# Performance work log

Hardware: AMD Instinct MI355X
Metric: run time of the kernel (lower is better)

The kernel has to match this reference:

```python
import jax, jax.numpy as jnp
import numpy as np

UFEAT_DIM = 512
EFEAT_DIM = 256
BATCH = 64
PNUM_UNIT = 1024
PNUM_ENEMY = 1024


def setup_inputs() -> dict:
    key = jax.random.key(0)
    k1, k2, k3, k4, k5 = jax.random.split(key, 5)
    ufeat = jax.random.normal(k1, (BATCH, PNUM_UNIT, UFEAT_DIM), dtype=jnp.float32)
    efeat = jax.random.normal(k2, (BATCH, PNUM_ENEMY, EFEAT_DIM), dtype=jnp.float32)
    num_enemy = jax.random.randint(k3, (BATCH,), 0, PNUM_ENEMY, dtype=jnp.int64)
    # weight_norm(Linear, dim=None): W = g * v / ||v||_F, g scalar
    v = jax.random.normal(k4, (EFEAT_DIM, UFEAT_DIM), dtype=jnp.float32) * (1.0 / np.sqrt(UFEAT_DIM))
    g = jnp.asarray(jnp.linalg.norm(v), dtype=jnp.float32)  # init g = ||v||
    b = jax.random.normal(k5, (EFEAT_DIM,), dtype=jnp.float32) * 0.01
    return {"ufeat": ufeat, "efeat": efeat, "num_enemy": num_enemy, "v": v, "g": g, "b": b}


def reference(ufeat, efeat, num_enemy, v, g, b):
    # weight-normed linear (dim=None -> Frobenius norm) + ReLU projection
    W = g * v / jnp.linalg.norm(v)                       # [efeat_dim, ufeat_dim]
    proj = jax.nn.relu(ufeat @ W.T + b)                  # [B, U, efeat_dim]
    # batched dot-product scores (fused matmul instead of repeat+mul+sum)
    norm = jnp.float32(np.sqrt(EFEAT_DIM))
    logit = jnp.einsum('bue,bne->bun', proj, efeat) / norm  # [B, U, N]
    # real-enemy mask: mask[b, n] = 1 iff n < num_enemy[b]
    mask = (jnp.arange(PNUM_ENEMY)[None, :] < num_enemy[:, None]).astype(logit.dtype)
    logit = logit - (1.0 - mask)[:, None, :] * 1e9       # masking bias (uniform if all masked)
    prob = jax.nn.softmax(logit, axis=2)
    return prob
```

## Files before the change

### kernel.cpp

```cpp
#include <hip/hip_runtime.h>
#include <hip/hip_bf16.h>

#define UF 512
#define EF 256
#define NB 64
#define NU 1024
#define NEN 1024

typedef __attribute__((ext_vector_type(8))) short short8;
typedef __attribute__((ext_vector_type(4))) float floatx4;

typedef unsigned short ushort_t;

__device__ inline short2 cvt2(float a, float b) {
    __hip_bfloat162 h = __float22bfloat162_rn(make_float2(a, b));
    union { __hip_bfloat162 h; short2 s; } u;
    u.h = h;
    return u.s;
}

__device__ inline short8 cvt8v(floatx4 x, floatx4 y) {
    union { short8 v; short2 s[4]; } u;
    u.s[0] = cvt2(x[0], x[1]);
    u.s[1] = cvt2(x[2], x[3]);
    u.s[2] = cvt2(y[0], y[1]);
    u.s[3] = cvt2(y[2], y[3]);
    return u.v;
}

__device__ inline ushort_t f2bfbits(float f) {
    unsigned u = __float_as_uint(f);
    u += 0x7FFFu + ((u >> 16) & 1u);
    return (ushort_t)(u >> 16);
}

__global__ void knorm(const float* __restrict__ v, float* __restrict__ ws0) {
    int t = blockIdx.x * 256 + threadIdx.x;
    float2 x = ((const float2*)v)[t];
    float s = x.x * x.x + x.y * x.y;
    #pragma unroll
    for (int m = 1; m < 64; m <<= 1) s += __shfl_xor(s, m);
    __shared__ float ls[4];
    int w = threadIdx.x >> 6;
    if ((threadIdx.x & 63) == 0) ls[w] = s;
    __syncthreads();
    if (threadIdx.x == 0) atomicAdd(ws0, ls[0] + ls[1] + ls[2] + ls[3]);
}

__global__ void kconv(const float* __restrict__ v, const float* __restrict__ g,
                      const float* __restrict__ ef, const float* __restrict__ ws0,
                      const int* __restrict__ nen,
                      ushort_t* __restrict__ wsW, ushort_t* __restrict__ wsE) {
    int bid = blockIdx.x;
    if (bid < 128) {
        int t = bid * 256 + threadIdx.x;
        float s = g[0] * rsqrtf(ws0[0]);
        float4 x = ((const float4*)v)[t];
        short2 a = cvt2(x.x * s, x.y * s);
        short2 b = cvt2(x.z * s, x.w * s);
        ushort4 o;
        o.x = (ushort_t)a.x; o.y = (ushort_t)a.y; o.z = (ushort_t)b.x; o.w = (ushort_t)b.y;
        ((ushort4*)wsW)[t] = o;
    } else {
        long t = (long)(bid - 128) * 256 + threadIdx.x;
        int row = (int)(t >> 6);
        int n = row & (NEN - 1);
        int b = row >> 10;
        if (n < nen[b]) {
            floatx4 x = __builtin_nontemporal_load((const floatx4*)ef + t);
            short2 a = cvt2(x[0], x[1]);
            short2 c = cvt2(x[2], x[3]);
            ushort4 o;
            o.x = (ushort_t)a.x; o.y = (ushort_t)a.y; o.z = (ushort_t)c.x; o.w = (ushort_t)c.y;
            ((ushort4*)wsE)[t] = o;
        }
    }
}

__launch_bounds__(256, 2)
__global__ void kfused(const float* __restrict__ A, const ushort_t* __restrict__ W,
                       const float* __restrict__ bias, const ushort_t* __restrict__ E,
                       const int* __restrict__ nen, float* __restrict__ out) {
    const int tid = threadIdx.x;
    const int w = tid >> 6, L = tid & 63;
    const int rA = L & 15, q = L >> 4;
    const int bid = blockIdx.x;
    const int b = bid >> 5;
    const int ut = bid & 31;
    const int ne = nen[b];

    __shared__ ushort_t Pl[32][256];
    __shared__ float lsum[4][32];

    {
        const long m0 = (long)b * NU + (long)ut * 32;
        floatx4 acc[2][4];
        #pragma unroll
        for (int m = 0; m < 2; m++)
            #pragma unroll
            for (int n = 0; n < 4; n++) acc[m][n] = (floatx4){0.f, 0.f, 0.f, 0.f};

        const float* a0 = A + (m0 + rA) * UF + q * 8;
        const float* a1 = A + (m0 + 16 + rA) * UF + q * 8;
        const ushort_t* wp[4];
        #pragma unroll
        for (int n = 0; n < 4; n++) wp[n] = W + (long)(w * 64 + n * 16 + rA) * UF + q * 8;

        floatx4 x0 = *(const floatx4*)(a0);
        floatx4 y0 = *(const floatx4*)(a0 + 4);
        floatx4 x1 = *(const floatx4*)(a1);
        floatx4 y1 = *(const floatx4*)(a1 + 4);

        #pragma unroll 2
        for (int s = 0; s < 16; s++) {
            const int ko = s * 32;
            short8 wf[4];
            #pragma unroll
            for (int n = 0; n < 4; n++) wf[n] = *(const short8*)(wp[n] + ko);
            short8 af0 = cvt8v(x0, y0);
            short8 af1 = cvt8v(x1, y1);
            if (s < 15) {
                x0 = *(const floatx4*)(a0 + ko + 32);
                y0 = *(const floatx4*)(a0 + ko + 36);
                x1 = *(const floatx4*)(a1 + ko + 32);
                y1 = *(const floatx4*)(a1 + ko + 36);
            }
            #pragma unroll
            for (int n = 0; n < 4; n++) {
                acc[0][n] = __builtin_amdgcn_mfma_f32_16x16x32_bf16(af0, wf[n], acc[0][n], 0, 0, 0);
                acc[1][n] = __builtin_amdgcn_mfma_f32_16x16x32_bf16(af1, wf[n], acc[1][n], 0, 0, 0);
            }
        }

        #pragma unroll
        for (int n = 0; n < 4; n++) {
            const int col = w * 64 + n * 16 + rA;
            const float bv = bias[col];
            #pragma unroll
            for (int m = 0; m < 2; m++) {
                #pragma unroll
                for (int i = 0; i < 4; i++) {
                    float val = acc[m][n][i] + bv;
                    val = fmaxf(val, 0.f);
                    Pl[m * 16 + q * 4 + i][col] = f2bfbits(val);
                }
            }
        }
    }
    __syncthreads();

    short8 af[2][8];
    #pragma unroll
    for (int t = 0; t < 2; t++)
        #pragma unroll
        for (int s = 0; s < 8; s++)
            af[t][s] = *(const short8*)&Pl[t * 16 + rA][s * 32 + q * 8];

    floatx4 acc[2][16];
    #pragma unroll
    for (int t = 0; t < 2; t++)
        #pragma unroll
        for (int ns = 0; ns < 16; ns++) acc[t][ns] = (floatx4){0.f, 0.f, 0.f, 0.f};
    float psum[2][4];
    #pragma unroll
    for (int t = 0; t < 2; t++)
        #pragma unroll
        for (int i = 0; i < 4; i++) psum[t][i] = 0.f;

    const ushort_t* erow = E + (long)(b * NEN + w * 16 + rA) * EF + q * 8;

    #pragma unroll
    for (int ns = 0; ns < 16; ns++) {
        const int col0 = ns * 64 + w * 16;
        if (col0 < ne) {
            const ushort_t* ep = erow + (long)ns * 64 * EF;
            floatx4 c0 = (floatx4){0.f, 0.f, 0.f, 0.f};
            floatx4 c1 = (floatx4){0.f, 0.f, 0.f, 0.f};
            #pragma unroll
            for (int h = 0; h < 2; h++) {
                short8 bf[4];
                #pragma unroll
                for (int s = 0; s < 4; s++) bf[s] = *(const short8*)(ep + (h * 4 + s) * 32);
                #pragma unroll
                for (int s = 0; s < 4; s++) {
                    c0 = __builtin_amdgcn_mfma_f32_16x16x32_bf16(af[0][h * 4 + s], bf[s], c0, 0, 0, 0);
                    c1 = __builtin_amdgcn_mfma_f32_16x16x32_bf16(af[1][h * 4 + s], bf[s], c1, 0, 0, 0);
                }
            }
            const int col = col0 + rA;
            const bool on = col < ne;
            #pragma unroll
            for (int i = 0; i < 4; i++) {
                float e0 = on ? __expf(c0[i] * 0.0625f) : 0.f;
                float e1 = on ? __expf(c1[i] * 0.0625f) : 0.f;
                c0[i] = e0; c1[i] = e1;
                psum[0][i] += e0; psum[1][i] += e1;
            }
            acc[0][ns] = c0;
            acc[1][ns] = c1;
        }
    }

    #pragma unroll
    for (int t = 0; t < 2; t++)
        #pragma unroll
        for (int i = 0; i < 4; i++) {
            float s = psum[t][i];
            s += __shfl_xor(s, 1);
            s += __shfl_xor(s, 2);
            s += __shfl_xor(s, 4);
            s += __shfl_xor(s, 8);
            psum[t][i] = s;
        }
    if (rA == 0) {
        #pragma unroll
        for (int t = 0; t < 2; t++)
            #pragma unroll
            for (int i = 0; i < 4; i++)
                lsum[w][t * 16 + q * 4 + i] = psum[t][i];
    }
    __syncthreads();

    float inv[2][4];
    #pragma unroll
    for (int t = 0; t < 2; t++)
        #pragma unroll
        for (int i = 0; i < 4; i++) {
            const int r = t * 16 + q * 4 + i;
            const float tot = lsum[0][r] + lsum[1][r] + lsum[2][r] + lsum[3][r];
            inv[t][i] = (ne > 0) ? (1.f / tot) : 0.f;
        }

    const float uni = 1.f / 1024.f;
    float* orow = out + ((long)(b * NU + ut * 32)) * (long)NEN + w * 16;
    #pragma unroll
    for (int ns = 0; ns < 16; ns++) {
        #pragma unroll
        for (int t = 0; t < 2; t++) {
            #pragma unroll
            for (int i = 0; i < 4; i++) {
                const int u = t * 16 + q * 4 + i;
                const float val = (ne == 0) ? uni : acc[t][ns][i] * inv[t][i];
                __builtin_nontemporal_store(val, &orow[(long)u * NEN + ns * 64 + rA]);
            }
        }
    }
}

extern "C" void kernel_launch(void* const* d_in, const int* in_sizes, int n_in,
                              void* d_out, int out_size, void* d_ws, size_t ws_size,
                              hipStream_t stream) {
    (void)in_sizes; (void)n_in; (void)out_size; (void)ws_size;
    const float* ufeat = (const float*)d_in[0];
    const float* efeat = (const float*)d_in[1];
    const int*   nen   = (const int*)d_in[2];
    const float* v     = (const float*)d_in[3];
    const float* g     = (const float*)d_in[4];
    const float* bias  = (const float*)d_in[5];
    float* out = (float*)d_out;

    float*    ws0 = (float*)d_ws;
    ushort_t* wsW = (ushort_t*)((char*)d_ws + 1024);
    ushort_t* wsE = (ushort_t*)((char*)d_ws + (1u << 20));

    hipMemsetAsync(d_ws, 0, 256, stream);
    knorm<<<256, 256, 0, stream>>>(v, ws0);
    kconv<<<16512, 256, 0, stream>>>(v, g, efeat, ws0, nen, wsW, wsE);
    kfused<<<2048, 256, 0, stream>>>(ufeat, wsW, bias, wsE, nen, out);
}
```

Measured before the change: 569.2 us.

## Store exp accumulators as fp16, double-buffer E loads, pad LDS rows

The kernel now keeps the per-tile exponentiated scores in packed fp16 pairs instead of fp32, halving that register array so the E-operand loads can be double-buffered: the next tile's B fragments are prefetched while the current tile's MFMAs run. The LDS projection buffer is padded from 256 to 264 columns to cut bank conflicts on the fragment reads. The fp16 numerators lose precision, and because the max is never subtracted, unmasked exp values can overflow the fp16 range.

```diff
diff --git a/kernel.cpp b/kernel.cpp
--- a/kernel.cpp
+++ b/kernel.cpp
@@ -9,6 +9,7 @@
 
 typedef __attribute__((ext_vector_type(8))) short short8;
 typedef __attribute__((ext_vector_type(4))) float floatx4;
+typedef __attribute__((ext_vector_type(2))) _Float16 half2v;
 
 typedef unsigned short ushort_t;
 
@@ -89,7 +90,7 @@
     const int ut = bid & 31;
     const int ne = nen[b];
 
-    __shared__ ushort_t Pl[32][256];
+    __shared__ ushort_t Pl[32][264];
     __shared__ float lsum[4][32];
 
     {
@@ -156,11 +157,14 @@
         for (int s = 0; s < 8; s++)
             af[t][s] = *(const short8*)&Pl[t * 16 + rA][s * 32 + q * 8];
 
-    floatx4 acc[2][16];
-    #pragma unroll
-    for (int t = 0; t < 2; t++)
-        #pragma unroll
-        for (int ns = 0; ns < 16; ns++) acc[t][ns] = (floatx4){0.f, 0.f, 0.f, 0.f};
+    half2v acc[2][16][2];
+    #pragma unroll
+    for (int t = 0; t < 2; t++)
+        #pragma unroll
+        for (int ns = 0; ns < 16; ns++) {
+            acc[t][ns][0] = (half2v){(_Float16)0.f, (_Float16)0.f};
+            acc[t][ns][1] = (half2v){(_Float16)0.f, (_Float16)0.f};
+        }
     float psum[2][4];
     #pragma unroll
     for (int t = 0; t < 2; t++)
@@ -168,24 +172,29 @@
         for (int i = 0; i < 4; i++) psum[t][i] = 0.f;
 
     const ushort_t* erow = E + (long)(b * NEN + w * 16 + rA) * EF + q * 8;
+
+    short8 bf[2][8];
+    if (w * 16 < ne) {
+        #pragma unroll
+        for (int s = 0; s < 8; s++) bf[0][s] = *(const short8*)(erow + s * 32);
+    }
 
     #pragma unroll
     for (int ns = 0; ns < 16; ns++) {
         const int col0 = ns * 64 + w * 16;
         if (col0 < ne) {
-            const ushort_t* ep = erow + (long)ns * 64 * EF;
+            const int cur = ns & 1;
+            if (ns < 15) {
+                const ushort_t* epn = erow + (long)(ns + 1) * 64 * EF;
+                #pragma unroll
+                for (int s = 0; s < 8; s++) bf[cur ^ 1][s] = *(const short8*)(epn + s * 32);
+            }
             floatx4 c0 = (floatx4){0.f, 0.f, 0.f, 0.f};
             floatx4 c1 = (floatx4){0.f, 0.f, 0.f, 0.f};
             #pragma unroll
-            for (int h = 0; h < 2; h++) {
-                short8 bf[4];
-                #pragma unroll
-                for (int s = 0; s < 4; s++) bf[s] = *(const short8*)(ep + (h * 4 + s) * 32);
-                #pragma unroll
-                for (int s = 0; s < 4; s++) {
-                    c0 = __builtin_amdgcn_mfma_f32_16x16x32_bf16(af[0][h * 4 + s], bf[s], c0, 0, 0, 0);
-                    c1 = __builtin_amdgcn_mfma_f32_16x16x32_bf16(af[1][h * 4 + s], bf[s], c1, 0, 0, 0);
-                }
+            for (int s = 0; s < 8; s++) {
+                c0 = __builtin_amdgcn_mfma_f32_16x16x32_bf16(af[0][s], bf[cur][s], c0, 0, 0, 0);
+                c1 = __builtin_amdgcn_mfma_f32_16x16x32_bf16(af[1][s], bf[cur][s], c1, 0, 0, 0);
             }
             const int col = col0 + rA;
             const bool on = col < ne;
@@ -193,11 +202,13 @@
             for (int i = 0; i < 4; i++) {
                 float e0 = on ? __expf(c0[i] * 0.0625f) : 0.f;
                 float e1 = on ? __expf(c1[i] * 0.0625f) : 0.f;
+                psum[0][i] += e0; psum[1][i] += e1;
                 c0[i] = e0; c1[i] = e1;
-                psum[0][i] += e0; psum[1][i] += e1;
-            }
-            acc[0][ns] = c0;
-            acc[1][ns] = c1;
+            }
+            acc[0][ns][0] = (half2v){(_Float16)c0[0], (_Float16)c0[1]};
+            acc[0][ns][1] = (half2v){(_Float16)c0[2], (_Float16)c0[3]};
+            acc[1][ns][0] = (half2v){(_Float16)c1[0], (_Float16)c1[1]};
+            acc[1][ns][1] = (half2v){(_Float16)c1[2], (_Float16)c1[3]};
         }
     }
 
@@ -240,7 +251,8 @@
             #pragma unroll
             for (int i = 0; i < 4; i++) {
                 const int u = t * 16 + q * 4 + i;
-                const float val = (ne == 0) ? uni : acc[t][ns][i] * inv[t][i];
+                const float num = (float)acc[t][ns][i >> 1][i & 1];
+                const float val = (ne == 0) ? uni : num * inv[t][i];
                 __builtin_nontemporal_store(val, &orow[(long)u * NEN + ns * 64 + rA]);
             }
         }
```

Measured after the change: 563.7 us. About the same (-1.0%).

## Halve row tile, store exp values as fp16, and stage output through LDS

Applied to the files above, without the earlier changes.

The fused kernel now processes 16 user rows per block instead of 32, doubling the grid and raising the launch-bounds occupancy target to 4 blocks per CU. Exponentiated scores are held as fp16 pairs to cut register pressure. Output is written through a shared-memory staging buffer, so each wave issues coalesced 16-byte nontemporal stores instead of scattered scalar ones. The trade-offs are that each E tile is now reloaded by twice as many blocks, fp16 storage loses precision on the unnormalized exp values, and the staging adds barriers.

```diff
diff --git a/kernel.cpp b/kernel.cpp
--- a/kernel.cpp
+++ b/kernel.cpp
@@ -9,6 +9,7 @@
 
 typedef __attribute__((ext_vector_type(8))) short short8;
 typedef __attribute__((ext_vector_type(4))) float floatx4;
+typedef __attribute__((ext_vector_type(2))) _Float16 half2v;
 
 typedef unsigned short ushort_t;
 
@@ -77,7 +78,7 @@
     }
 }
 
-__launch_bounds__(256, 2)
+__launch_bounds__(256, 4)
 __global__ void kfused(const float* __restrict__ A, const ushort_t* __restrict__ W,
                        const float* __restrict__ bias, const ushort_t* __restrict__ E,
                        const int* __restrict__ nen, float* __restrict__ out) {
@@ -85,31 +86,29 @@
     const int w = tid >> 6, L = tid & 63;
     const int rA = L & 15, q = L >> 4;
     const int bid = blockIdx.x;
-    const int b = bid >> 5;
-    const int ut = bid & 31;
+    const int b = bid >> 6;
+    const int ut = bid & 63;
     const int ne = nen[b];
 
-    __shared__ ushort_t Pl[32][256];
-    __shared__ float lsum[4][32];
+    __shared__ union ShMem {
+        ushort_t Pl[16][264];
+        float    Cl[16][260];
+    } sh;
+    __shared__ float lsum[4][16];
 
     {
-        const long m0 = (long)b * NU + (long)ut * 32;
-        floatx4 acc[2][4];
-        #pragma unroll
-        for (int m = 0; m < 2; m++)
-            #pragma unroll
-            for (int n = 0; n < 4; n++) acc[m][n] = (floatx4){0.f, 0.f, 0.f, 0.f};
+        const long m0 = (long)b * NU + (long)ut * 16;
+        floatx4 acc[4];
+        #pragma unroll
+        for (int n = 0; n < 4; n++) acc[n] = (floatx4){0.f, 0.f, 0.f, 0.f};
 
         const float* a0 = A + (m0 + rA) * UF + q * 8;
-        const float* a1 = A + (m0 + 16 + rA) * UF + q * 8;
         const ushort_t* wp[4];
         #pragma unroll
         for (int n = 0; n < 4; n++) wp[n] = W + (long)(w * 64 + n * 16 + rA) * UF + q * 8;
 
         floatx4 x0 = *(const floatx4*)(a0);
         floatx4 y0 = *(const floatx4*)(a0 + 4);
-        floatx4 x1 = *(const floatx4*)(a1);
-        floatx4 y1 = *(const floatx4*)(a1 + 4);
 
         #pragma unroll 2
         for (int s = 0; s < 16; s++) {
@@ -118,18 +117,13 @@
             #pragma unroll
             for (int n = 0; n < 4; n++) wf[n] = *(const short8*)(wp[n] + ko);
             short8 af0 = cvt8v(x0, y0);
-            short8 af1 = cvt8v(x1, y1);
             if (s < 15) {
                 x0 = *(const floatx4*)(a0 + ko + 32);
                 y0 = *(const floatx4*)(a0 + ko + 36);
-                x1 = *(const floatx4*)(a1 + ko + 32);
-                y1 = *(const floatx4*)(a1 + ko + 36);
-            }
-            #pragma unroll
-            for (int n = 0; n < 4; n++) {
-                acc[0][n] = __builtin_amdgcn_mfma_f32_16x16x32_bf16(af0, wf[n], acc[0][n], 0, 0, 0);
-                acc[1][n] = __builtin_amdgcn_mfma_f32_16x16x32_bf16(af1, wf[n], acc[1][n], 0, 0, 0);
-            }
+            }
+            #pragma unroll
+            for (int n = 0; n < 4; n++)
+                acc[n] = __builtin_amdgcn_mfma_f32_16x16x32_bf16(af0, wf[n], acc[n], 0, 0, 0);
         }
 
         #pragma unroll
@@ -137,35 +131,27 @@
             const int col = w * 64 + n * 16 + rA;
             const float bv = bias[col];
             #pragma unroll
-            for (int m = 0; m < 2; m++) {
-                #pragma unroll
-                for (int i = 0; i < 4; i++) {
-                    float val = acc[m][n][i] + bv;
-                    val = fmaxf(val, 0.f);
-                    Pl[m * 16 + q * 4 + i][col] = f2bfbits(val);
-                }
+            for (int i = 0; i < 4; i++) {
+                float val = acc[n][i] + bv;
+                val = fmaxf(val, 0.f);
+                sh.Pl[q * 4 + i][col] = f2bfbits(val);
             }
         }
     }
     __syncthreads();
 
-    short8 af[2][8];
-    #pragma unroll
-    for (int t = 0; t < 2; t++)
-        #pragma unroll
-        for (int s = 0; s < 8; s++)
-            af[t][s] = *(const short8*)&Pl[t * 16 + rA][s * 32 + q * 8];
-
-    floatx4 acc[2][16];
-    #pragma unroll
-    for (int t = 0; t < 2; t++)
-        #pragma unroll
-        for (int ns = 0; ns < 16; ns++) acc[t][ns] = (floatx4){0.f, 0.f, 0.f, 0.f};
-    float psum[2][4];
-    #pragma unroll
-    for (int t = 0; t < 2; t++)
-        #pragma unroll
-        for (int i = 0; i < 4; i++) psum[t][i] = 0.f;
+    short8 af[8];
+    #pragma unroll
+    for (int s = 0; s < 8; s++)
+        af[s] = *(const short8*)&sh.Pl[rA][s * 32 + q * 8];
+
+    half2v acc[16][2];
+    #pragma unroll
+    for (int ns = 0; ns < 16; ns++) {
+        acc[ns][0] = (half2v){(_Float16)0.f, (_Float16)0.f};
+        acc[ns][1] = (half2v){(_Float16)0.f, (_Float16)0.f};
+    }
+    float psum[4] = {0.f, 0.f, 0.f, 0.f};
 
     const ushort_t* erow = E + (long)(b * NEN + w * 16 + rA) * EF + q * 8;
 
@@ -174,75 +160,71 @@
         const int col0 = ns * 64 + w * 16;
         if (col0 < ne) {
             const ushort_t* ep = erow + (long)ns * 64 * EF;
+            short8 bf[8];
+            #pragma unroll
+            for (int s = 0; s < 8; s++) bf[s] = *(const short8*)(ep + s * 32);
             floatx4 c0 = (floatx4){0.f, 0.f, 0.f, 0.f};
-            floatx4 c1 = (floatx4){0.f, 0.f, 0.f, 0.f};
-            #pragma unroll
-            for (int h = 0; h < 2; h++) {
-                short8 bf[4];
-                #pragma unroll
-                for (int s = 0; s < 4; s++) bf[s] = *(const short8*)(ep + (h * 4 + s) * 32);
-                #pragma unroll
-                for (int s = 0; s < 4; s++) {
-                    c0 = __builtin_amdgcn_mfma_f32_16x16x32_bf16(af[0][h * 4 + s], bf[s], c0, 0, 0, 0);
-                    c1 = __builtin_amdgcn_mfma_f32_16x16x32_bf16(af[1][h * 4 + s], bf[s], c1, 0, 0, 0);
-                }
-            }
+            #pragma unroll
+            for (int s = 0; s < 8; s++)
+                c0 = __builtin_amdgcn_mfma_f32_16x16x32_bf16(af[s], bf[s], c0, 0, 0, 0);
             const int col = col0 + rA;
             const bool on = col < ne;
             #pragma unroll
             for (int i = 0; i < 4; i++) {
                 float e0 = on ? __expf(c0[i] * 0.0625f) : 0.f;
-                float e1 = on ? __expf(c1[i] * 0.0625f) : 0.f;
-                c0[i] = e0; c1[i] = e1;
-                psum[0][i] += e0; psum[1][i] += e1;
-            }
-            acc[0][ns] = c0;
-            acc[1][ns] = c1;
-        }
-    }
-
-    #pragma unroll
-    for (int t = 0; t < 2; t++)
-        #pragma unroll
-        for (int i = 0; i < 4; i++) {
-            float s = psum[t][i];
-            s += __shfl_xor(s, 1);
-            s += __shfl_xor(s, 2);
-            s += __shfl_xor(s, 4);
-            s += __shfl_xor(s, 8);
-            psum[t][i] = s;
-        }
+                psum[i] += e0;
+                c0[i] = e0;
+            }
+            acc[ns][0] = (half2v){(_Float16)c0[0], (_Float16)c0[1]};
+            acc[ns][1] = (half2v){(_Float16)c0[2], (_Float16)c0[3]};
+        }
+    }
+
+    #pragma unroll
+    for (int i = 0; i < 4; i++) {
+        float s = psum[i];
+        s += __shfl_xor(s, 1);
+        s += __shfl_xor(s, 2);
+        s += __shfl_xor(s, 4);
+        s += __shfl_xor(s, 8);
+        psum[i] = s;
+    }
     if (rA == 0) {
         #pragma unroll
-        for (int t = 0; t < 2; t++)
-            #pragma unroll
-            for (int i = 0; i < 4; i++)
-                lsum[w][t * 16 + q * 4 + i] = psum[t][i];
+        for (int i = 0; i < 4; i++) lsum[w][q * 4 + i] = psum[i];
     }
     __syncthreads();
 
-    float inv[2][4];
-    #pragma unroll
-    for (int t = 0; t < 2; t++)
-        #pragma unroll
-        for (int i = 0; i < 4; i++) {
-            const int r = t * 16 + q * 4 + i;
-            const float tot = lsum[0][r] + lsum[1][r] + lsum[2][r] + lsum[3][r];
-            inv[t][i] = (ne > 0) ? (1.f / tot) : 0.f;
-        }
+    float inv[4];
+    #pragma unroll
+    for (int i = 0; i < 4; i++) {
+        const int r = q * 4 + i;
+        const float tot = lsum[0][r] + lsum[1][r] + lsum[2][r] + lsum[3][r];
+        inv[i] = (ne > 0) ? (1.f / tot) : 0.f;
+    }
 
     const float uni = 1.f / 1024.f;
-    float* orow = out + ((long)(b * NU + ut * 32)) * (long)NEN + w * 16;
-    #pragma unroll
-    for (int ns = 0; ns < 16; ns++) {
-        #pragma unroll
-        for (int t = 0; t < 2; t++) {
+    const long obase = ((long)(b * NU + ut * 16)) * (long)NEN;
+    #pragma unroll
+    for (int g = 0; g < 4; g++) {
+        if (g > 0) __syncthreads();
+        #pragma unroll
+        for (int ns2 = 0; ns2 < 4; ns2++) {
+            const int ns = g * 4 + ns2;
             #pragma unroll
             for (int i = 0; i < 4; i++) {
-                const int u = t * 16 + q * 4 + i;
-                const float val = (ne == 0) ? uni : acc[t][ns][i] * inv[t][i];
-                __builtin_nontemporal_store(val, &orow[(long)u * NEN + ns * 64 + rA]);
-            }
+                const float num = (float)acc[ns][i >> 1][i & 1];
+                const float val = (ne == 0) ? uni : num * inv[i];
+                sh.Cl[q * 4 + i][ns2 * 64 + w * 16 + rA] = val;
+            }
+        }
+        __syncthreads();
+        #pragma unroll
+        for (int j = 0; j < 4; j++) {
+            const int r = w * 4 + j;
+            floatx4 vv = *(const floatx4*)&sh.Cl[r][L * 4];
+            __builtin_nontemporal_store(vv,
+                (floatx4*)(out + obase + (long)r * NEN + g * 256 + L * 4));
         }
     }
 }
@@ -266,5 +248,5 @@
     hipMemsetAsync(d_ws, 0, 256, stream);
     knorm<<<256, 256, 0, stream>>>(v, ws0);
     kconv<<<16512, 256, 0, stream>>>(v, g, efeat, ws0, nen, wsW, wsE);
-    kfused<<<2048, 256, 0, stream>>>(ufeat, wsW, bias, wsE, nen, out);
-}
+    kfused<<<4096, 256, 0, stream>>>(ufeat, wsW, bias, wsE, nen, out);
+}
```

New measurement: 681.8 us. +19.8%, slower.
